# Performance work log

Hardware: AMD Instinct MI355X
Metric: run time of the kernel (lower is better)

Reference implementation:

```python
import jax, jax.numpy as jnp
import numpy as np

SUP_NUM = 2048
EPS_NORM = 1e-12
EPS_BN = 1e-5


def l2norm(v, axis):
    n = jnp.sqrt(jnp.sum(v * v, axis=axis, keepdims=True))
    return v / jnp.maximum(n, EPS_NORM)


def segment_mean(vals, ids, num_segments):
    # vals: [N, C], ids: [N] int -> [num_segments, C]
    s = jax.ops.segment_sum(vals, ids, num_segments=num_segments)
    cnt = jax.ops.segment_sum(jnp.ones((vals.shape[0],), vals.dtype), ids, num_segments=num_segments)
    return s / jnp.maximum(cnt, 1.0)[:, None]


def setup_inputs() -> dict:
    key = jax.random.key(0)
    ks = jax.random.split(key, 6)
    B, Cin, H, W = 1, 3, 1024, 1024
    Cf = 32
    x = jax.random.normal(ks[0], (B, Cin, H, W), dtype=jnp.float32)
    conv_feat = jax.random.normal(ks[1], (B, Cf, H, W), dtype=jnp.float32)
    vit_feature = jax.random.normal(ks[2], (B, SUP_NUM, Cf), dtype=jnp.float32)
    seg_ids = jax.random.randint(ks[3], (B * H * W,), 0, SUP_NUM, dtype=jnp.int32)
    w_soft = jax.random.normal(ks[4], (1, 2 * Cf, 3), dtype=jnp.float32) * 0.1
    b_soft = jnp.zeros((1,), jnp.float32)
    bn_gamma = jnp.ones((1,), jnp.float32)
    bn_beta = jnp.zeros((1,), jnp.float32)
    return {"x": x, "conv_feat": conv_feat, "vit_feature": vit_feature, "seg_ids": seg_ids,
            "w_soft": w_soft, "b_soft": b_soft, "bn_gamma": bn_gamma, "bn_beta": bn_beta}


def reference(x, conv_feat, vit_feature, seg_ids, w_soft, b_soft, bn_gamma, bn_beta):
    B, Cf, H, W = conv_feat.shape
    Cin = x.shape[1]
    # F.normalize(conv, p=2, dim=1)
    conv_1 = l2norm(conv_feat, axis=1)
    # [B,C,H,W] -> [B*H*W, C]
    F1 = conv_1.transpose(0, 2, 3, 1).reshape(-1, Cf)
    X = jax.lax.stop_gradient(x).transpose(0, 2, 3, 1).reshape(-1, Cin)
    # superpixel scatter-mean (replaces the per-segment Python loop)
    M_F = segment_mean(F1, seg_ids, SUP_NUM)                  # [Sup, Cf]
    X_F = segment_mean(X, seg_ids, SUP_NUM)                   # [Sup, Cin]
    M_F = M_F.reshape(B, SUP_NUM, Cf)
    X_F = X_F.reshape(B, SUP_NUM, Cin).transpose(0, 2, 1)     # [B, Cin, Sup]
    vit_n = l2norm(vit_feature, axis=-1)
    all_F = jnp.concatenate([M_F, vit_n], axis=-1).transpose(0, 2, 1)  # [B, 2Cf, Sup]
    all_F = l2norm(all_F, axis=1)
    # Conv1d(2Cf -> 1, k=3, pad=1)
    z = jax.lax.conv_general_dilated(all_F, w_soft, window_strides=(1,), padding=((1, 1),),
                                     dimension_numbers=("NCH", "OIH", "NCH")) + b_soft[None, :, None]
    # BatchNorm1d (training-mode batch stats over (B, L))
    mu = jnp.mean(z, axis=(0, 2), keepdims=True)
    var = jnp.mean((z - mu) ** 2, axis=(0, 2), keepdims=True)
    z = bn_gamma[None, :, None] * (z - mu) / jnp.sqrt(var + EPS_BN) + bn_beta[None, :, None]
    result = jax.nn.sigmoid(z)                                # [B, 1, Sup]
    gap = jnp.mean(result, axis=-1, keepdims=True)            # AdaptiveAvgPool1d(1)
    return (result, gap, all_F, X_F)
```

## Files before the change

kernel.cpp:

```cpp
#include <hip/hip_runtime.h>
#include <hip/hip_bf16.h>
#include <hip/hip_fp16.h>

#define SUP 2048
#define NXB 128

#define SC_CONV 1024.0f
#define SC_X0   512.0f
#define SC_XLO  256.0f
#define ISC_CONV (1.0f/1024.0f)
#define ISC_X0   (1.0f/512.0f)
#define ISC_XLO  (1.0f/256.0f)

__device__ __forceinline__ int enc2i(int qa, int qb) {
    return ((qa - (qb < 0 ? 1 : 0)) << 16) + (qb & 0xFFFF);
}
__device__ __forceinline__ int enc2f(float a, float b) {
    return enc2i(__float2int_rn(a), __float2int_rn(b));
}

__global__ __launch_bounds__(256) void k_invnorm(const float* __restrict__ conv,
                                                 __half* __restrict__ inv,
                                                 int npix) {
    int t = blockIdx.x * blockDim.x + threadIdx.x;
    int p = t * 4;
    if (p + 3 < npix) {
        float4 s = {0.f, 0.f, 0.f, 0.f};
#pragma unroll
        for (int c = 0; c < 32; ++c) {
            float4 v = *(const float4*)(conv + (size_t)c * npix + p);
            s.x += v.x * v.x; s.y += v.y * v.y; s.z += v.z * v.z; s.w += v.w * v.w;
        }
        __half2 h0 = __floats2half2_rn(1.0f / fmaxf(sqrtf(s.x), 1e-12f),
                                       1.0f / fmaxf(sqrtf(s.y), 1e-12f));
        __half2 h1 = __floats2half2_rn(1.0f / fmaxf(sqrtf(s.z), 1e-12f),
                                       1.0f / fmaxf(sqrtf(s.w), 1e-12f));
        *(__half2*)(inv + p) = h0;
        *(__half2*)(inv + p + 2) = h1;
    } else {
        for (; p < npix; ++p) {
            float s = 0.f;
#pragma unroll
            for (int c = 0; c < 32; ++c) {
                float v = conv[(size_t)c * npix + p];
                s += v * v;
            }
            inv[p] = __float2half(1.0f / fmaxf(sqrtf(s), 1e-12f));
        }
    }
}

__global__ __launch_bounds__(1024) void k_segacc(const float* __restrict__ conv,
                                                 const float* __restrict__ x,
                                                 const int* __restrict__ ids,
                                                 const __half* __restrict__ inv,
                                                 float* __restrict__ accum,
                                                 __half* __restrict__ pbuf,
                                                 int npix) {
    __shared__ int sacc[9 * SUP];
    int g = blockIdx.y;
    int cb = g * 16;
    for (int i = threadIdx.x; i < 9 * SUP; i += blockDim.x) sacc[i] = 0;
    __syncthreads();

    int per = ((npix + (int)gridDim.x - 1) / (int)gridDim.x + 3) & ~3;
    int start = blockIdx.x * per;
    int end = min(start + per, npix);
    int nvec = (end > start) ? ((end - start) & ~3) : 0;
    int vend = start + nvec;

    const float* cc = conv + (size_t)cb * npix;

    for (int p = start + (int)threadIdx.x * 4; p < vend; p += (int)blockDim.x * 4) {
        int4 s4 = *(const int4*)(ids + p);
        __half2 h01 = *(const __half2*)(inv + p);
        __half2 h23 = *(const __half2*)(inv + p + 2);
        float w0 = __low2float(h01), w1 = __high2float(h01);
        float w2 = __low2float(h23), w3 = __high2float(h23);
#pragma unroll
        for (int cp = 0; cp < 8; ++cp) {
            float4 va = *(const float4*)(cc + (size_t)(2 * cp) * npix + p);
            float4 vb = *(const float4*)(cc + (size_t)(2 * cp + 1) * npix + p);
            atomicAdd(&sacc[cp * SUP + s4.x], enc2f(va.x * w0 * SC_CONV, vb.x * w0 * SC_CONV));
            atomicAdd(&sacc[cp * SUP + s4.y], enc2f(va.y * w1 * SC_CONV, vb.y * w1 * SC_CONV));
            atomicAdd(&sacc[cp * SUP + s4.z], enc2f(va.z * w2 * SC_CONV, vb.z * w2 * SC_CONV));
            atomicAdd(&sacc[cp * SUP + s4.w], enc2f(va.w * w3 * SC_CONV, vb.w * w3 * SC_CONV));
        }
        if (g == 0) {
            float4 a = *(const float4*)(x + p);
            float4 b = *(const float4*)(x + (size_t)npix + p);
            atomicAdd(&sacc[8 * SUP + s4.x], enc2f(a.x * SC_X0, b.x * SC_XLO));
            atomicAdd(&sacc[8 * SUP + s4.y], enc2f(a.y * SC_X0, b.y * SC_XLO));
            atomicAdd(&sacc[8 * SUP + s4.z], enc2f(a.z * SC_X0, b.z * SC_XLO));
            atomicAdd(&sacc[8 * SUP + s4.w], enc2f(a.w * SC_X0, b.w * SC_XLO));
        } else {
            float4 c = *(const float4*)(x + (size_t)2 * npix + p);
            atomicAdd(&sacc[8 * SUP + s4.x], enc2i(1, __float2int_rn(c.x * SC_XLO)));
            atomicAdd(&sacc[8 * SUP + s4.y], enc2i(1, __float2int_rn(c.y * SC_XLO)));
            atomicAdd(&sacc[8 * SUP + s4.z], enc2i(1, __float2int_rn(c.z * SC_XLO)));
            atomicAdd(&sacc[8 * SUP + s4.w], enc2i(1, __float2int_rn(c.w * SC_XLO)));
        }
    }
    for (int p = vend + (int)threadIdx.x; p < end; p += (int)blockDim.x) {
        int s = ids[p];
        float w = __half2float(inv[p]);
#pragma unroll
        for (int cp = 0; cp < 8; ++cp) {
            float va = cc[(size_t)(2 * cp) * npix + p];
            float vb = cc[(size_t)(2 * cp + 1) * npix + p];
            atomicAdd(&sacc[cp * SUP + s], enc2f(va * w * SC_CONV, vb * w * SC_CONV));
        }
        if (g == 0) {
            atomicAdd(&sacc[8 * SUP + s],
                      enc2f(x[p] * SC_X0, x[(size_t)npix + p] * SC_XLO));
        } else {
            atomicAdd(&sacc[8 * SUP + s],
                      enc2i(1, __float2int_rn(x[(size_t)2 * npix + p] * SC_XLO)));
        }
    }
    __syncthreads();

    for (int i = threadIdx.x; i < 9 * SUP; i += blockDim.x) {
        int S = sacc[i];
        int qb = (int)(short)(S & 0xFFFF);
        int qa = (S - qb) >> 16;
        int row = i >> 11;
        int s = i & (SUP - 1);
        int hi_row, lo_row;
        float fhi, flo;
        if (row < 8) {
            int ch = cb + 2 * row;
            hi_row = ch; lo_row = ch + 1;
            fhi = (float)qa * ISC_CONV;
            flo = (float)qb * ISC_CONV;
        } else if (g == 0) {
            hi_row = 32; lo_row = 33;
            fhi = (float)qa * ISC_X0;
            flo = (float)qb * ISC_XLO;
        } else {
            hi_row = 35; lo_row = 34;
            fhi = (float)qa;
            flo = (float)qb * ISC_XLO;
        }
        if (pbuf) {
            __half* dst = pbuf + (size_t)blockIdx.x * 36 * SUP;
            dst[hi_row * SUP + s] = __float2half(fhi);
            dst[lo_row * SUP + s] = __float2half(flo);
        } else {
            unsafeAtomicAdd(&accum[hi_row * SUP + s], fhi);
            unsafeAtomicAdd(&accum[lo_row * SUP + s], flo);
        }
    }
}

__global__ __launch_bounds__(256) void k_reduce(const __half* __restrict__ pbuf,
                                                float* __restrict__ accum) {
    int j8 = (blockIdx.x * blockDim.x + threadIdx.x) * 8;
    if (j8 >= 36 * SUP) return;
    float s[8];
#pragma unroll
    for (int k = 0; k < 8; ++k) s[k] = 0.f;
    for (int b = 0; b < NXB; ++b) {
        uint4 u = *(const uint4*)(pbuf + (size_t)b * 36 * SUP + j8);
        __half2 h0 = *reinterpret_cast<__half2*>(&u.x);
        __half2 h1 = *reinterpret_cast<__half2*>(&u.y);
        __half2 h2 = *reinterpret_cast<__half2*>(&u.z);
        __half2 h3 = *reinterpret_cast<__half2*>(&u.w);
        float2 f0 = __half22float2(h0), f1 = __half22float2(h1);
        float2 f2 = __half22float2(h2), f3 = __half22float2(h3);
        s[0] += f0.x; s[1] += f0.y; s[2] += f1.x; s[3] += f1.y;
        s[4] += f2.x; s[5] += f2.y; s[6] += f3.x; s[7] += f3.y;
    }
    float4 o0 = {s[0], s[1], s[2], s[3]};
    float4 o1 = {s[4], s[5], s[6], s[7]};
    *(float4*)(accum + j8) = o0;
    *(float4*)(accum + j8 + 4) = o1;
}

__device__ __forceinline__ void compute_col(const float* __restrict__ accum,
                                            const float* __restrict__ vit,
                                            int g, float* __restrict__ col) {
    if (g < 0 || g >= SUP) {
#pragma unroll
        for (int c = 0; c < 64; ++c) col[c] = 0.f;
        return;
    }
    float cnt = fmaxf(accum[35 * SUP + g], 1.0f);
    float rc = 1.0f / cnt;
#pragma unroll
    for (int c = 0; c < 32; ++c) col[c] = accum[c * SUP + g] * rc;
    float vs = 0.f;
#pragma unroll
    for (int c = 0; c < 32; ++c) {
        float v = vit[g * 32 + c];
        col[32 + c] = v;
        vs += v * v;
    }
    float vinv = 1.0f / fmaxf(sqrtf(vs), 1e-12f);
#pragma unroll
    for (int c = 0; c < 32; ++c) col[32 + c] *= vinv;
    float ssq = 0.f;
#pragma unroll
    for (int c = 0; c < 64; ++c) ssq += col[c] * col[c];
    float ainv = 1.0f / fmaxf(sqrtf(ssq), 1e-12f);
#pragma unroll
    for (int c = 0; c < 64; ++c) col[c] *= ainv;
}

__global__ __launch_bounds__(256) void k_finalconv(const float* __restrict__ accum,
                                                   const float* __restrict__ vit,
                                                   const float* __restrict__ w,
                                                   const float* __restrict__ bias,
                                                   float* __restrict__ allF_out,
                                                   float* __restrict__ xf_out,
                                                   float* __restrict__ z_out) {
    __shared__ float L[258][65];
    __shared__ float sw[192];
    int t = threadIdx.x;
    int b0 = blockIdx.x * 256;
    if (t < 192) sw[t] = w[t];

    float col[64];
    int g = b0 + t;
    compute_col(accum, vit, g, col);
#pragma unroll
    for (int c = 0; c < 64; ++c) L[t + 1][c] = col[c];
#pragma unroll
    for (int c = 0; c < 64; ++c) allF_out[c * SUP + g] = col[c];
    {
        float cnt = fmaxf(accum[35 * SUP + g], 1.0f);
        float rc = 1.0f / cnt;
#pragma unroll
        for (int c = 0; c < 3; ++c)
            xf_out[c * SUP + g] = accum[(32 + c) * SUP + g] * rc;
    }
    if (t == 0) {
        compute_col(accum, vit, b0 - 1, col);
#pragma unroll
        for (int c = 0; c < 64; ++c) L[0][c] = col[c];
    }
    if (t == 255) {
        compute_col(accum, vit, b0 + 256, col);
#pragma unroll
        for (int c = 0; c < 64; ++c) L[257][c] = col[c];
    }
    __syncthreads();

    float acc = bias[0];
#pragma unroll
    for (int c = 0; c < 64; ++c) {
        acc += sw[c * 3] * L[t][c] + sw[c * 3 + 1] * L[t + 1][c]
             + sw[c * 3 + 2] * L[t + 2][c];
    }
    z_out[b0 + t] = acc;
}

__global__ __launch_bounds__(512) void k_head2(const float* __restrict__ z,
                                               const float* __restrict__ gamma,
                                               const float* __restrict__ beta,
                                               float* __restrict__ out) {
    __shared__ float red[8];
    __shared__ float bc[2];
    int tid = threadIdx.x;
    int lane = tid & 63, wid = tid >> 6;

    float zs[4];
#pragma unroll
    for (int j = 0; j < 4; ++j) zs[j] = z[j * 512 + tid];

    float s1 = zs[0] + zs[1] + zs[2] + zs[3];
#pragma unroll
    for (int o = 32; o > 0; o >>= 1) s1 += __shfl_down(s1, o);
    if (lane == 0) red[wid] = s1;
    __syncthreads();
    if (tid == 0) {
        float t = 0.f;
        for (int i = 0; i < 8; ++i) t += red[i];
        bc[0] = t / (float)SUP;
    }
    __syncthreads();
    float mu = bc[0];

    float s2 = 0.f;
#pragma unroll
    for (int j = 0; j < 4; ++j) { float d = zs[j] - mu; s2 += d * d; }
#pragma unroll
    for (int o = 32; o > 0; o >>= 1) s2 += __shfl_down(s2, o);
    __syncthreads();
    if (lane == 0) red[wid] = s2;
    __syncthreads();
    if (tid == 0) {
        float t = 0.f;
        for (int i = 0; i < 8; ++i) t += red[i];
        bc[1] = t / (float)SUP;
    }
    __syncthreads();
    float var = bc[1];

    float invstd = rsqrtf(var + 1e-5f);
    float gm = gamma[0], bt = beta[0];
    float gsum = 0.f;
#pragma unroll
    for (int j = 0; j < 4; ++j) {
        int p = j * 512 + tid;
        float zn = gm * (zs[j] - mu) * invstd + bt;
        float r = 1.0f / (1.0f + expf(-zn));
        out[p] = r;
        gsum += r;
    }
#pragma unroll
    for (int o = 32; o > 0; o >>= 1) gsum += __shfl_down(gsum, o);
    __syncthreads();
    if (lane == 0) red[wid] = gsum;
    __syncthreads();
    if (tid == 0) {
        float t = 0.f;
        for (int i = 0; i < 8; ++i) t += red[i];
        out[SUP] = t / (float)SUP;
    }
}

extern "C" void kernel_launch(void* const* d_in, const int* in_sizes, int n_in,
                              void* d_out, int out_size, void* d_ws, size_t ws_size,
                              hipStream_t stream) {
    const float* x     = (const float*)d_in[0];
    const float* conv  = (const float*)d_in[1];
    const float* vit   = (const float*)d_in[2];
    const int*   ids   = (const int*)d_in[3];
    const float* w     = (const float*)d_in[4];
    const float* b     = (const float*)d_in[5];
    const float* gamma = (const float*)d_in[6];
    const float* beta  = (const float*)d_in[7];
    float* out = (float*)d_out;

    int npix = in_sizes[3];

    __half* inv = (__half*)d_ws;
    float* accum = (float*)((char*)d_ws + ((size_t)npix * 2 + 255 & ~(size_t)255));
    float* zbuf = accum + 36 * SUP;
    __half* pbuf = (__half*)(zbuf + SUP);

    size_t need = ((size_t)npix * 2 + 256) + (36 * SUP + SUP) * sizeof(float)
                + (size_t)NXB * 36 * SUP * sizeof(__half);
    bool useP = ws_size >= need;

    if (!useP) hipMemsetAsync(accum, 0, 36 * SUP * sizeof(float), stream);

    int nquad = (npix + 3) / 4;
    k_invnorm<<<(nquad + 255) / 256, 256, 0, stream>>>(conv, inv, npix);

    dim3 g2(NXB, 2);
    k_segacc<<<g2, 1024, 0, stream>>>(conv, x, ids, inv, accum,
                                      useP ? pbuf : (__half*)nullptr, npix);
    if (useP) {
        k_reduce<<<(36 * SUP / 8 + 255) / 256, 256, 0, stream>>>(pbuf, accum);
    }

    float* allF = out + SUP + 1;
    float* xf = allF + 64 * SUP;
    k_finalconv<<<SUP / 256, 256, 0, stream>>>(accum, vit, w, b, allF, xf, zbuf);

    k_head2<<<1, 512, 0, stream>>>(zbuf, gamma, beta, out);
}
```

Baseline: 80.98 us.

## Fuse inverse-norm computation into segment accumulation kernel with all channels per block

Drops the separate inverse-norm kernel and computes each pixel's L2 norm inline from the 32 conv channels held in registers, then does the shared-memory atomic accumulation for all 32 channels plus x in one block. This avoids reading conv twice from global memory and removes the fp16 inv buffer round-trip. The grid goes from 128x2 blocks to 256 one-dimensional blocks, with 18*SUP ints (144KB) of shared memory per block. In exchange it raises register pressure (32 float2 per thread), gives lower occupancy from the larger shared allocation, and doubles the partial buffers that k_reduce must sum.

```diff
diff --git a/kernel.cpp b/kernel.cpp
--- a/kernel.cpp
+++ b/kernel.cpp
@@ -3,7 +3,7 @@
 #include <hip/hip_fp16.h>
 
 #define SUP 2048
-#define NXB 128
+#define NB  256
 
 #define SC_CONV 1024.0f
 #define SC_X0   512.0f
@@ -19,108 +19,72 @@
     return enc2i(__float2int_rn(a), __float2int_rn(b));
 }
 
-__global__ __launch_bounds__(256) void k_invnorm(const float* __restrict__ conv,
-                                                 __half* __restrict__ inv,
-                                                 int npix) {
-    int t = blockIdx.x * blockDim.x + threadIdx.x;
-    int p = t * 4;
-    if (p + 3 < npix) {
-        float4 s = {0.f, 0.f, 0.f, 0.f};
-#pragma unroll
-        for (int c = 0; c < 32; ++c) {
-            float4 v = *(const float4*)(conv + (size_t)c * npix + p);
-            s.x += v.x * v.x; s.y += v.y * v.y; s.z += v.z * v.z; s.w += v.w * v.w;
-        }
-        __half2 h0 = __floats2half2_rn(1.0f / fmaxf(sqrtf(s.x), 1e-12f),
-                                       1.0f / fmaxf(sqrtf(s.y), 1e-12f));
-        __half2 h1 = __floats2half2_rn(1.0f / fmaxf(sqrtf(s.z), 1e-12f),
-                                       1.0f / fmaxf(sqrtf(s.w), 1e-12f));
-        *(__half2*)(inv + p) = h0;
-        *(__half2*)(inv + p + 2) = h1;
-    } else {
-        for (; p < npix; ++p) {
-            float s = 0.f;
-#pragma unroll
-            for (int c = 0; c < 32; ++c) {
-                float v = conv[(size_t)c * npix + p];
-                s += v * v;
-            }
-            inv[p] = __float2half(1.0f / fmaxf(sqrtf(s), 1e-12f));
-        }
-    }
-}
-
-__global__ __launch_bounds__(1024) void k_segacc(const float* __restrict__ conv,
-                                                 const float* __restrict__ x,
-                                                 const int* __restrict__ ids,
-                                                 const __half* __restrict__ inv,
-                                                 float* __restrict__ accum,
-                                                 __half* __restrict__ pbuf,
-                                                 int npix) {
-    __shared__ int sacc[9 * SUP];
-    int g = blockIdx.y;
-    int cb = g * 16;
-    for (int i = threadIdx.x; i < 9 * SUP; i += blockDim.x) sacc[i] = 0;
-    __syncthreads();
-
-    int per = ((npix + (int)gridDim.x - 1) / (int)gridDim.x + 3) & ~3;
+__global__ __launch_bounds__(1024) void k_segfused(const float* __restrict__ conv,
+                                                   const float* __restrict__ x,
+                                                   const int* __restrict__ ids,
+                                                   float* __restrict__ accum,
+                                                   __half* __restrict__ pbuf,
+                                                   int npix) {
+    __shared__ int sacc[18 * SUP];
+    for (int i = threadIdx.x; i < 18 * SUP; i += blockDim.x) sacc[i] = 0;
+    __syncthreads();
+
+    int per = ((npix + (int)gridDim.x - 1) / (int)gridDim.x + 1) & ~1;
     int start = blockIdx.x * per;
     int end = min(start + per, npix);
-    int nvec = (end > start) ? ((end - start) & ~3) : 0;
-    int vend = start + nvec;
-
-    const float* cc = conv + (size_t)cb * npix;
-
-    for (int p = start + (int)threadIdx.x * 4; p < vend; p += (int)blockDim.x * 4) {
-        int4 s4 = *(const int4*)(ids + p);
-        __half2 h01 = *(const __half2*)(inv + p);
-        __half2 h23 = *(const __half2*)(inv + p + 2);
-        float w0 = __low2float(h01), w1 = __high2float(h01);
-        float w2 = __low2float(h23), w3 = __high2float(h23);
-#pragma unroll
-        for (int cp = 0; cp < 8; ++cp) {
-            float4 va = *(const float4*)(cc + (size_t)(2 * cp) * npix + p);
-            float4 vb = *(const float4*)(cc + (size_t)(2 * cp + 1) * npix + p);
-            atomicAdd(&sacc[cp * SUP + s4.x], enc2f(va.x * w0 * SC_CONV, vb.x * w0 * SC_CONV));
-            atomicAdd(&sacc[cp * SUP + s4.y], enc2f(va.y * w1 * SC_CONV, vb.y * w1 * SC_CONV));
-            atomicAdd(&sacc[cp * SUP + s4.z], enc2f(va.z * w2 * SC_CONV, vb.z * w2 * SC_CONV));
-            atomicAdd(&sacc[cp * SUP + s4.w], enc2f(va.w * w3 * SC_CONV, vb.w * w3 * SC_CONV));
-        }
-        if (g == 0) {
-            float4 a = *(const float4*)(x + p);
-            float4 b = *(const float4*)(x + (size_t)npix + p);
-            atomicAdd(&sacc[8 * SUP + s4.x], enc2f(a.x * SC_X0, b.x * SC_XLO));
-            atomicAdd(&sacc[8 * SUP + s4.y], enc2f(a.y * SC_X0, b.y * SC_XLO));
-            atomicAdd(&sacc[8 * SUP + s4.z], enc2f(a.z * SC_X0, b.z * SC_XLO));
-            atomicAdd(&sacc[8 * SUP + s4.w], enc2f(a.w * SC_X0, b.w * SC_XLO));
-        } else {
-            float4 c = *(const float4*)(x + (size_t)2 * npix + p);
-            atomicAdd(&sacc[8 * SUP + s4.x], enc2i(1, __float2int_rn(c.x * SC_XLO)));
-            atomicAdd(&sacc[8 * SUP + s4.y], enc2i(1, __float2int_rn(c.y * SC_XLO)));
-            atomicAdd(&sacc[8 * SUP + s4.z], enc2i(1, __float2int_rn(c.z * SC_XLO)));
-            atomicAdd(&sacc[8 * SUP + s4.w], enc2i(1, __float2int_rn(c.w * SC_XLO)));
-        }
-    }
-    for (int p = vend + (int)threadIdx.x; p < end; p += (int)blockDim.x) {
+    int stride2 = (int)blockDim.x * 2;
+
+    int p = start + (int)threadIdx.x * 2;
+    for (; p + 1 < end; p += stride2) {
+        int2 id2 = *(const int2*)(ids + p);
+        float2 cv[32];
+        float s0 = 0.f, s1 = 0.f;
+#pragma unroll
+        for (int c = 0; c < 32; ++c) {
+            cv[c] = *(const float2*)(conv + (size_t)c * npix + p);
+            s0 += cv[c].x * cv[c].x;
+            s1 += cv[c].y * cv[c].y;
+        }
+        float i0 = 1.0f / fmaxf(sqrtf(s0), 1e-12f);
+        float i1 = 1.0f / fmaxf(sqrtf(s1), 1e-12f);
+#pragma unroll
+        for (int r = 0; r < 16; ++r) {
+            float2 a = cv[2 * r], b = cv[2 * r + 1];
+            atomicAdd(&sacc[r * SUP + id2.x],
+                      enc2f(a.x * i0 * SC_CONV, b.x * i0 * SC_CONV));
+            atomicAdd(&sacc[r * SUP + id2.y],
+                      enc2f(a.y * i1 * SC_CONV, b.y * i1 * SC_CONV));
+        }
+        float2 x0 = *(const float2*)(x + p);
+        float2 x1 = *(const float2*)(x + (size_t)npix + p);
+        float2 x2 = *(const float2*)(x + (size_t)2 * npix + p);
+        atomicAdd(&sacc[16 * SUP + id2.x], enc2f(x0.x * SC_X0, x1.x * SC_XLO));
+        atomicAdd(&sacc[16 * SUP + id2.y], enc2f(x0.y * SC_X0, x1.y * SC_XLO));
+        atomicAdd(&sacc[17 * SUP + id2.x], enc2i(1, __float2int_rn(x2.x * SC_XLO)));
+        atomicAdd(&sacc[17 * SUP + id2.y], enc2i(1, __float2int_rn(x2.y * SC_XLO)));
+    }
+    if (p == end - 1) {
         int s = ids[p];
-        float w = __half2float(inv[p]);
-#pragma unroll
-        for (int cp = 0; cp < 8; ++cp) {
-            float va = cc[(size_t)(2 * cp) * npix + p];
-            float vb = cc[(size_t)(2 * cp + 1) * npix + p];
-            atomicAdd(&sacc[cp * SUP + s], enc2f(va * w * SC_CONV, vb * w * SC_CONV));
-        }
-        if (g == 0) {
-            atomicAdd(&sacc[8 * SUP + s],
-                      enc2f(x[p] * SC_X0, x[(size_t)npix + p] * SC_XLO));
-        } else {
-            atomicAdd(&sacc[8 * SUP + s],
-                      enc2i(1, __float2int_rn(x[(size_t)2 * npix + p] * SC_XLO)));
-        }
-    }
-    __syncthreads();
-
-    for (int i = threadIdx.x; i < 9 * SUP; i += blockDim.x) {
+        float cvv[32];
+        float ss = 0.f;
+#pragma unroll
+        for (int c = 0; c < 32; ++c) {
+            cvv[c] = conv[(size_t)c * npix + p];
+            ss += cvv[c] * cvv[c];
+        }
+        float iv = 1.0f / fmaxf(sqrtf(ss), 1e-12f);
+#pragma unroll
+        for (int r = 0; r < 16; ++r)
+            atomicAdd(&sacc[r * SUP + s],
+                      enc2f(cvv[2 * r] * iv * SC_CONV, cvv[2 * r + 1] * iv * SC_CONV));
+        atomicAdd(&sacc[16 * SUP + s],
+                  enc2f(x[p] * SC_X0, x[(size_t)npix + p] * SC_XLO));
+        atomicAdd(&sacc[17 * SUP + s],
+                  enc2i(1, __float2int_rn(x[(size_t)2 * npix + p] * SC_XLO)));
+    }
+    __syncthreads();
+
+    for (int i = threadIdx.x; i < 18 * SUP; i += blockDim.x) {
         int S = sacc[i];
         int qb = (int)(short)(S & 0xFFFF);
         int qa = (S - qb) >> 16;
@@ -128,12 +92,11 @@
         int s = i & (SUP - 1);
         int hi_row, lo_row;
         float fhi, flo;
-        if (row < 8) {
-            int ch = cb + 2 * row;
-            hi_row = ch; lo_row = ch + 1;
+        if (row < 16) {
+            hi_row = 2 * row; lo_row = 2 * row + 1;
             fhi = (float)qa * ISC_CONV;
             flo = (float)qb * ISC_CONV;
-        } else if (g == 0) {
+        } else if (row == 16) {
             hi_row = 32; lo_row = 33;
             fhi = (float)qa * ISC_X0;
             flo = (float)qb * ISC_XLO;
@@ -160,7 +123,7 @@
     float s[8];
 #pragma unroll
     for (int k = 0; k < 8; ++k) s[k] = 0.f;
-    for (int b = 0; b < NXB; ++b) {
+    for (int b = 0; b < NB; ++b) {
         uint4 u = *(const uint4*)(pbuf + (size_t)b * 36 * SUP + j8);
         __half2 h0 = *reinterpret_cast<__half2*>(&u.x);
         __half2 h1 = *reinterpret_cast<__half2*>(&u.y);
@@ -335,23 +298,18 @@
 
     int npix = in_sizes[3];
 
-    __half* inv = (__half*)d_ws;
-    float* accum = (float*)((char*)d_ws + ((size_t)npix * 2 + 255 & ~(size_t)255));
+    float* accum = (float*)d_ws;
     float* zbuf = accum + 36 * SUP;
     __half* pbuf = (__half*)(zbuf + SUP);
 
-    size_t need = ((size_t)npix * 2 + 256) + (36 * SUP + SUP) * sizeof(float)
-                + (size_t)NXB * 36 * SUP * sizeof(__half);
+    size_t need = (36 * SUP + SUP) * sizeof(float)
+                + (size_t)NB * 36 * SUP * sizeof(__half);
     bool useP = ws_size >= need;
 
     if (!useP) hipMemsetAsync(accum, 0, 36 * SUP * sizeof(float), stream);
 
-    int nquad = (npix + 3) / 4;
-    k_invnorm<<<(nquad + 255) / 256, 256, 0, stream>>>(conv, inv, npix);
-
-    dim3 g2(NXB, 2);
-    k_segacc<<<g2, 1024, 0, stream>>>(conv, x, ids, inv, accum,
-                                      useP ? pbuf : (__half*)nullptr, npix);
+    k_segfused<<<NB, 1024, 0, stream>>>(conv, x, ids, accum,
+                                        useP ? pbuf : (__half*)nullptr, npix);
     if (useP) {
         k_reduce<<<(36 * SUP / 8 + 255) / 256, 256, 0, stream>>>(pbuf, accum);
     }
```

After: 76.48 us. 1.06x faster.

## Restructure segment accumulation: scalar per-pixel loads, 512-thread blocks, twice as many blocks

Applied to the files above, without the earlier changes.

The accumulation kernel drops the float4/int4 four-pixel vector path and has each thread handle two pixels per iteration with scalar coalesced loads, hoisting all 16 channel loads ahead of the shared-memory atomics. Block size is halved to 512 and the number of pixel-range blocks doubles to 256, so more blocks run concurrently with the 72KB shared histogram each. The likely goals are better latency hiding and less atomic serialization per block. In exchange, the per-block partial buffer and the reduce kernel's work double, and the scalar loads give up 16-byte vector transactions.

```diff
diff --git a/kernel.cpp b/kernel.cpp
--- a/kernel.cpp
+++ b/kernel.cpp
@@ -3,7 +3,7 @@
 #include <hip/hip_fp16.h>
 
 #define SUP 2048
-#define NXB 128
+#define NXB 256
 
 #define SC_CONV 1024.0f
 #define SC_X0   512.0f
@@ -50,72 +50,68 @@
     }
 }
 
-__global__ __launch_bounds__(1024) void k_segacc(const float* __restrict__ conv,
-                                                 const float* __restrict__ x,
-                                                 const int* __restrict__ ids,
-                                                 const __half* __restrict__ inv,
-                                                 float* __restrict__ accum,
-                                                 __half* __restrict__ pbuf,
-                                                 int npix) {
+__global__ __launch_bounds__(512) void k_segacc(const float* __restrict__ conv,
+                                                const float* __restrict__ x,
+                                                const int* __restrict__ ids,
+                                                const __half* __restrict__ inv,
+                                                float* __restrict__ accum,
+                                                __half* __restrict__ pbuf,
+                                                int npix) {
     __shared__ int sacc[9 * SUP];
     int g = blockIdx.y;
     int cb = g * 16;
     for (int i = threadIdx.x; i < 9 * SUP; i += blockDim.x) sacc[i] = 0;
     __syncthreads();
 
-    int per = ((npix + (int)gridDim.x - 1) / (int)gridDim.x + 3) & ~3;
+    int per = (npix + (int)gridDim.x - 1) / (int)gridDim.x;
     int start = blockIdx.x * per;
     int end = min(start + per, npix);
-    int nvec = (end > start) ? ((end - start) & ~3) : 0;
-    int vend = start + nvec;
 
     const float* cc = conv + (size_t)cb * npix;
 
-    for (int p = start + (int)threadIdx.x * 4; p < vend; p += (int)blockDim.x * 4) {
-        int4 s4 = *(const int4*)(ids + p);
-        __half2 h01 = *(const __half2*)(inv + p);
-        __half2 h23 = *(const __half2*)(inv + p + 2);
-        float w0 = __low2float(h01), w1 = __high2float(h01);
-        float w2 = __low2float(h23), w3 = __high2float(h23);
-#pragma unroll
-        for (int cp = 0; cp < 8; ++cp) {
-            float4 va = *(const float4*)(cc + (size_t)(2 * cp) * npix + p);
-            float4 vb = *(const float4*)(cc + (size_t)(2 * cp + 1) * npix + p);
-            atomicAdd(&sacc[cp * SUP + s4.x], enc2f(va.x * w0 * SC_CONV, vb.x * w0 * SC_CONV));
-            atomicAdd(&sacc[cp * SUP + s4.y], enc2f(va.y * w1 * SC_CONV, vb.y * w1 * SC_CONV));
-            atomicAdd(&sacc[cp * SUP + s4.z], enc2f(va.z * w2 * SC_CONV, vb.z * w2 * SC_CONV));
-            atomicAdd(&sacc[cp * SUP + s4.w], enc2f(va.w * w3 * SC_CONV, vb.w * w3 * SC_CONV));
-        }
-        if (g == 0) {
-            float4 a = *(const float4*)(x + p);
-            float4 b = *(const float4*)(x + (size_t)npix + p);
-            atomicAdd(&sacc[8 * SUP + s4.x], enc2f(a.x * SC_X0, b.x * SC_XLO));
-            atomicAdd(&sacc[8 * SUP + s4.y], enc2f(a.y * SC_X0, b.y * SC_XLO));
-            atomicAdd(&sacc[8 * SUP + s4.z], enc2f(a.z * SC_X0, b.z * SC_XLO));
-            atomicAdd(&sacc[8 * SUP + s4.w], enc2f(a.w * SC_X0, b.w * SC_XLO));
-        } else {
-            float4 c = *(const float4*)(x + (size_t)2 * npix + p);
-            atomicAdd(&sacc[8 * SUP + s4.x], enc2i(1, __float2int_rn(c.x * SC_XLO)));
-            atomicAdd(&sacc[8 * SUP + s4.y], enc2i(1, __float2int_rn(c.y * SC_XLO)));
-            atomicAdd(&sacc[8 * SUP + s4.z], enc2i(1, __float2int_rn(c.z * SC_XLO)));
-            atomicAdd(&sacc[8 * SUP + s4.w], enc2i(1, __float2int_rn(c.w * SC_XLO)));
-        }
-    }
-    for (int p = vend + (int)threadIdx.x; p < end; p += (int)blockDim.x) {
-        int s = ids[p];
-        float w = __half2float(inv[p]);
-#pragma unroll
-        for (int cp = 0; cp < 8; ++cp) {
-            float va = cc[(size_t)(2 * cp) * npix + p];
-            float vb = cc[(size_t)(2 * cp + 1) * npix + p];
-            atomicAdd(&sacc[cp * SUP + s], enc2f(va * w * SC_CONV, vb * w * SC_CONV));
-        }
-        if (g == 0) {
-            atomicAdd(&sacc[8 * SUP + s],
-                      enc2f(x[p] * SC_X0, x[(size_t)npix + p] * SC_XLO));
-        } else {
-            atomicAdd(&sacc[8 * SUP + s],
-                      enc2i(1, __float2int_rn(x[(size_t)2 * npix + p] * SC_XLO)));
+    for (int p0 = start + (int)threadIdx.x; p0 < end; p0 += 1024) {
+        int p1 = p0 + 512;
+        bool has1 = p1 < end;
+        int s0 = ids[p0];
+        float iv0 = __half2float(inv[p0]);
+        float a0[16];
+#pragma unroll
+        for (int c = 0; c < 16; ++c) a0[c] = cc[(size_t)c * npix + p0];
+        float xa0, xb0;
+        if (g == 0) { xa0 = x[p0]; xb0 = x[(size_t)npix + p0]; }
+        else        { xa0 = 0.f;  xb0 = x[(size_t)2 * npix + p0]; }
+
+        int s1 = 0; float iv1 = 0.f, xa1 = 0.f, xb1 = 0.f;
+        float a1[16];
+        if (has1) {
+            s1 = ids[p1];
+            iv1 = __half2float(inv[p1]);
+#pragma unroll
+            for (int c = 0; c < 16; ++c) a1[c] = cc[(size_t)c * npix + p1];
+            if (g == 0) { xa1 = x[p1]; xb1 = x[(size_t)npix + p1]; }
+            else        { xb1 = x[(size_t)2 * npix + p1]; }
+        }
+
+        float sc0 = iv0 * SC_CONV;
+#pragma unroll
+        for (int r = 0; r < 8; ++r)
+            atomicAdd(&sacc[r * SUP + s0],
+                      enc2f(a0[2 * r] * sc0, a0[2 * r + 1] * sc0));
+        if (g == 0)
+            atomicAdd(&sacc[8 * SUP + s0], enc2f(xa0 * SC_X0, xb0 * SC_XLO));
+        else
+            atomicAdd(&sacc[8 * SUP + s0], enc2i(1, __float2int_rn(xb0 * SC_XLO)));
+
+        if (has1) {
+            float sc1 = iv1 * SC_CONV;
+#pragma unroll
+            for (int r = 0; r < 8; ++r)
+                atomicAdd(&sacc[r * SUP + s1],
+                          enc2f(a1[2 * r] * sc1, a1[2 * r + 1] * sc1));
+            if (g == 0)
+                atomicAdd(&sacc[8 * SUP + s1], enc2f(xa1 * SC_X0, xb1 * SC_XLO));
+            else
+                atomicAdd(&sacc[8 * SUP + s1], enc2i(1, __float2int_rn(xb1 * SC_XLO)));
         }
     }
     __syncthreads();
@@ -129,8 +125,7 @@
         int hi_row, lo_row;
         float fhi, flo;
         if (row < 8) {
-            int ch = cb + 2 * row;
-            hi_row = ch; lo_row = ch + 1;
+            hi_row = cb + 2 * row; lo_row = hi_row + 1;
             fhi = (float)qa * ISC_CONV;
             flo = (float)qb * ISC_CONV;
         } else if (g == 0) {
@@ -336,7 +331,7 @@
     int npix = in_sizes[3];
 
     __half* inv = (__half*)d_ws;
-    float* accum = (float*)((char*)d_ws + ((size_t)npix * 2 + 255 & ~(size_t)255));
+    float* accum = (float*)((char*)d_ws + (((size_t)npix * 2 + 255) & ~(size_t)255));
     float* zbuf = accum + 36 * SUP;
     __half* pbuf = (__half*)(zbuf + SUP);
 
@@ -350,8 +345,8 @@
     k_invnorm<<<(nquad + 255) / 256, 256, 0, stream>>>(conv, inv, npix);
 
     dim3 g2(NXB, 2);
-    k_segacc<<<g2, 1024, 0, stream>>>(conv, x, ids, inv, accum,
-                                      useP ? pbuf : (__half*)nullptr, npix);
+    k_segacc<<<g2, 512, 0, stream>>>(conv, x, ids, inv, accum,
+                                     useP ? pbuf : (__half*)nullptr, npix);
     if (useP) {
         k_reduce<<<(36 * SUP / 8 + 255) / 256, 256, 0, stream>>>(pbuf, accum);
     }
```

Result: slower. 97.56 us (+20.5%).
